# Performance work log

Measured on AMD Instinct MI355X. Metric: run time of the kernel, lower is better.

The kernel has to match this reference:

```python
import jax, jax.numpy as jnp
import numpy as np

SCALE = 20.0
THRESHOLD = 0.9995


def setup_inputs() -> dict:
    key = jax.random.key(0)
    k1, k2, k3 = jax.random.split(key, 3)
    B, C, H, W, S = 4, 128, 96, 128, 1024
    # L2-normalize along channel so the dot product is a true cosine in [-1, 1]
    # (keeps exp(scale * (x - threshold)) numerically sane, as intended by the module).
    def unit(x):
        return x / (jnp.linalg.norm(x, axis=1, keepdims=True) + 1e-8)
    source_feature_map = unit(jax.random.normal(k1, (B, C, H, W), dtype=jnp.float32))
    target_feature_map = unit(jax.random.normal(k2, (B, C, H, W), dtype=jnp.float32))
    source_feature_1D_locations = jax.random.randint(k3, (B, S, 1), 0, H * W, dtype=jnp.int64)
    mask = jnp.ones((B, 1, H, W), dtype=jnp.float32)
    return {
        "source_feature_map": source_feature_map,
        "target_feature_map": target_feature_map,
        "source_feature_1D_locations": source_feature_1D_locations,
        "mask": mask,
    }


def reference(source_feature_map, target_feature_map, source_feature_1D_locations, mask):
    B, C, H, W = source_feature_map.shape
    loc = source_feature_1D_locations[..., 0]  # [B, S]
    src_flat = source_feature_map.reshape(B, C, H * W)  # [B, C, HW]
    # gather sampled query vectors: [B, C, S]
    sampled = jnp.take_along_axis(src_flat, loc[:, None, :], axis=2)
    # per-batch 1x1 conv == batched matmul: [B, S, H, W]
    corr = jnp.einsum('bchw,bcs->bshw', target_feature_map, sampled)
    resp = jnp.exp(SCALE * (0.5 * corr + 0.5 - THRESHOLD)) * mask  # mask broadcasts [B,1,H,W]
    resp = resp / jnp.sum(resp, axis=(2, 3), keepdims=True)
    return resp
```

## Files before the change

### kernel.cpp

```cpp
#include <hip/hip_runtime.h>

typedef unsigned int u32;
typedef unsigned short u16;
typedef short s8v __attribute__((ext_vector_type(8)));
typedef float f16v __attribute__((ext_vector_type(16)));
typedef _Float16 h8 __attribute__((ext_vector_type(8)));

#define NB 4
#define NC 128
#define HW 12288
#define NS 1024

#define EXP_A 10.0f
#define EXP_B (-9.99f)
#define ESCALE 4096.0f

#define TSR 128
#define TP 256
#define NPT (HW/TP)
#define NRT ((NB*NS)/TSR)

__device__ inline u16 f2bf(float f) {
    u32 u = __float_as_uint(f);
    return (u16)((u + 0x7fffu + ((u >> 16) & 1u)) >> 16);
}
__device__ inline float bf2f(u16 h) { return __uint_as_float(((u32)h) << 16); }

__device__ inline void gload_lds16(const void* g, void* l) {
    __builtin_amdgcn_global_load_lds(
        (const __attribute__((address_space(1))) void*)g,
        (__attribute__((address_space(3))) void*)l, 16, 0, 0);
}

__global__ __launch_bounds__(256) void prep(
    const float* __restrict__ src, const float* __restrict__ tgt,
    const int* __restrict__ loc,
    u16* __restrict__ ahi, u16* __restrict__ alo,
    u16* __restrict__ bhi, u16* __restrict__ blo,
    float* __restrict__ sums)
{
    int blk = blockIdx.x, t = threadIdx.x;
    if (blk < (HW / 64) * NB) {
        int b = blk / (HW / 64), pt = blk - b * (HW / 64);
        int pxl = t & 63, u = t >> 6;
        int px = pt * 64 + pxl;
        int slot = u ^ ((px >> 1) & 3);
#pragma unroll
        for (int kc = 0; kc < 4; ++kc) {
            int c0 = kc * 32 + u * 8;
            u32 hq[4], lq[4];
#pragma unroll
            for (int k = 0; k < 4; ++k) {
                float v0 = tgt[((size_t)(b * NC + c0 + 2 * k)) * HW + px];
                float v1 = tgt[((size_t)(b * NC + c0 + 2 * k + 1)) * HW + px];
                u16 h0 = f2bf(v0), h1 = f2bf(v1);
                u16 l0 = f2bf(v0 - bf2f(h0)), l1 = f2bf(v1 - bf2f(h1));
                hq[k] = (u32)h0 | ((u32)h1 << 16);
                lq[k] = (u32)l0 | ((u32)l1 << 16);
            }
            size_t off = (((size_t)((b * 4 + kc) * HW + px)) * 4 + slot) * 8;
            *(uint4*)(bhi + off) = make_uint4(hq[0], hq[1], hq[2], hq[3]);
            *(uint4*)(blo + off) = make_uint4(lq[0], lq[1], lq[2], lq[3]);
        }
    } else {
        int sb = blk - (HW / 64) * NB;
        int gid = sb * 256 + t;
        if (gid < NB * NS) sums[gid] = 0.0f;
        int bs = sb * 2 + (t >> 7);
        int c  = t & 127;
        int b  = bs >> 10, s = bs & 1023;
        int l  = loc[bs];
        float v = src[((size_t)(b * NC + c)) * HW + l];
        u16 h  = f2bf(v);
        u16 lo = f2bf(v - bf2f(h));
        int kc = c >> 5, u = (c >> 3) & 3, e = c & 7;
        int slot = u ^ ((s >> 1) & 3);
        size_t off = ((size_t)((b * 4 + kc) * NS + s)) * 32 + slot * 8 + e;
        ahi[off] = h;
        alo[off] = lo;
    }
}

template <int F16>
__global__ __launch_bounds__(256, 2) void corr_fused(
    const u16* __restrict__ bhi, const u16* __restrict__ blo,
    const u16* __restrict__ ahi, const u16* __restrict__ alo,
    const float* __restrict__ mask, float* __restrict__ sums,
    _Float16* __restrict__ ebuf, float* __restrict__ out)
{
    __shared__ __align__(1024) char sm[49152];

    int f = blockIdx.x;
    int xcd = f & 7, r = f >> 3;
    int pt = xcd * 6 + (r >> 5);
    int rt = r & 31;
    int b  = rt >> 3, st2 = rt & 7;

    int t = threadIdx.x, w = t >> 6, l = t & 63, ln = l & 31, h = l >> 5;
    int ws = w >> 1, wp = w & 1;

    f16v acc[2][4];
#pragma unroll
    for (int i = 0; i < 2; ++i)
#pragma unroll
        for (int j = 0; j < 4; ++j)
#pragma unroll
            for (int r2 = 0; r2 < 16; ++r2) acc[i][j][r2] = 0.0f;

    for (int kc = 0; kc < 4; ++kc) {
        const char* ga_h = (const char*)ahi + ((size_t)((b * 4 + kc) * NS + st2 * TSR)) * 64;
        const char* ga_l = (const char*)alo + ((size_t)((b * 4 + kc) * NS + st2 * TSR)) * 64;
        const char* gb_h = (const char*)bhi + ((size_t)((b * 4 + kc) * HW + pt * TP)) * 64;
        const char* gb_l = (const char*)blo + ((size_t)((b * 4 + kc) * HW + pt * TP)) * 64;
#pragma unroll
        for (int it = 0; it < 12; ++it) {
            int q = w * 12 + it;
            const char* g; int inner;
            if (q < 8)       { g = ga_h; inner = q; }
            else if (q < 16) { g = ga_l; inner = q - 8; }
            else if (q < 32) { g = gb_h; inner = q - 16; }
            else             { g = gb_l; inner = q - 32; }
            gload_lds16(g + inner * 1024 + l * 16, sm + q * 1024);
        }
        __syncthreads();

#pragma unroll
        for (int kk2 = 0; kk2 < 2; ++kk2) {
            int u = kk2 * 2 + h;
            s8v a_h[2], a_l[2], b_h[4], b_l[4];
#pragma unroll
            for (int i = 0; i < 2; ++i) {
                int row = ws * 64 + i * 32 + ln;
                int sl = u ^ ((row >> 1) & 3);
                a_h[i] = *(const s8v*)(sm + 0 * 8192 + row * 64 + sl * 16);
                a_l[i] = *(const s8v*)(sm + 1 * 8192 + row * 64 + sl * 16);
            }
#pragma unroll
            for (int j = 0; j < 4; ++j) {
                int px = wp * 128 + j * 32 + ln;
                int sl = u ^ ((px >> 1) & 3);
                b_h[j] = *(const s8v*)(sm + 16384 + px * 64 + sl * 16);
                b_l[j] = *(const s8v*)(sm + 32768 + px * 64 + sl * 16);
            }
            __builtin_amdgcn_s_setprio(1);
#pragma unroll
            for (int i = 0; i < 2; ++i)
#pragma unroll
                for (int j = 0; j < 4; ++j) {
                    acc[i][j] = __builtin_amdgcn_mfma_f32_32x32x16_bf16(a_h[i], b_h[j], acc[i][j], 0, 0, 0);
                    acc[i][j] = __builtin_amdgcn_mfma_f32_32x32x16_bf16(a_l[i], b_h[j], acc[i][j], 0, 0, 0);
                    acc[i][j] = __builtin_amdgcn_mfma_f32_32x32x16_bf16(a_h[i], b_l[j], acc[i][j], 0, 0, 0);
                }
            __builtin_amdgcn_s_setprio(0);
        }
        __syncthreads();
    }

    float mvs[4];
#pragma unroll
    for (int j = 0; j < 4; ++j)
        mvs[j] = mask[(size_t)b * HW + pt * TP + wp * 128 + j * 32 + ln] * ESCALE;

    float* rs = (float*)sm;
    size_t base = ((size_t)(b * NS + st2 * TSR)) * HW + pt * TP + wp * 128 + ln;
    _Float16* eb0 = ebuf + base;
    float*    ob0 = out  + base;
#pragma unroll
    for (int i = 0; i < 2; ++i) {
        int rb = ws * 64 + i * 32 + 4 * h;
#pragma unroll
        for (int r2 = 0; r2 < 16; ++r2) {
            int row = rb + (r2 & 3) + 8 * (r2 >> 2);
            float tot = 0.0f;
#pragma unroll
            for (int j = 0; j < 4; ++j) {
                float e = __expf(fmaf(acc[i][j][r2], EXP_A, EXP_B)) * mvs[j];
                if (F16) eb0[(size_t)row * HW + j * 32] = (_Float16)e;
                else     ob0[(size_t)row * HW + j * 32] = e;
                tot += e;
            }
            rs[(wp * TSR + row) * 32 + ln] = tot;
        }
    }
    __syncthreads();
    int row2 = t & 127, half = t >> 7;
    float tot = 0.0f;
#pragma unroll
    for (int c = 0; c < 32; ++c)
        tot += rs[(half * TSR + row2) * 32 + ((c + t) & 31)];
    atomicAdd(&sums[b * NS + st2 * TSR + row2], tot);
}

__global__ __launch_bounds__(256) void rescale16(
    const float* __restrict__ sums, const _Float16* __restrict__ ebuf,
    float* __restrict__ out)
{
    int bs = blockIdx.x;
    float inv = 1.0f / sums[bs];
    const h8* p = (const h8*)(ebuf + (size_t)bs * HW);
    float4* o = (float4*)(out + (size_t)bs * HW);
    int t = threadIdx.x;
#pragma unroll
    for (int i = 0; i < 6; ++i) {
        int idx = t + i * 256;
        h8 v = p[idx];
        float4 a, c;
        a.x = (float)v[0] * inv; a.y = (float)v[1] * inv;
        a.z = (float)v[2] * inv; a.w = (float)v[3] * inv;
        c.x = (float)v[4] * inv; c.y = (float)v[5] * inv;
        c.z = (float)v[6] * inv; c.w = (float)v[7] * inv;
        o[2 * idx]     = a;
        o[2 * idx + 1] = c;
    }
}

__global__ __launch_bounds__(256) void rescale32(
    const float* __restrict__ sums, float* __restrict__ out)
{
    int bs = blockIdx.x;
    float inv = 1.0f / sums[bs];
    float4* p = (float4*)(out + (size_t)bs * HW);
    int t = threadIdx.x;
#pragma unroll
    for (int i = 0; i < 12; ++i) {
        float4 v = p[t + i * 256];
        v.x *= inv; v.y *= inv; v.z *= inv; v.w *= inv;
        p[t + i * 256] = v;
    }
}

extern "C" void kernel_launch(void* const* d_in, const int* in_sizes, int n_in,
                              void* d_out, int out_size, void* d_ws, size_t ws_size,
                              hipStream_t stream) {
    const float* src  = (const float*)d_in[0];
    const float* tgt  = (const float*)d_in[1];
    const int*   loc  = (const int*)d_in[2];
    const float* mask = (const float*)d_in[3];
    float* out = (float*)d_out;

    char* ws = (char*)d_ws;
    const size_t BPLANE = (size_t)NB * 4 * HW * 32 * sizeof(u16);
    const size_t APLANE = (size_t)NB * 4 * NS * 32 * sizeof(u16);
    const size_t EPLANE = (size_t)NB * NS * HW * sizeof(_Float16);
    u16* bhi = (u16*)ws;
    u16* blo = (u16*)(ws + BPLANE);
    u16* ahi = (u16*)(ws + 2 * BPLANE);
    u16* alo = (u16*)(ws + 2 * BPLANE + APLANE);
    float* sums = (float*)(ws + 2 * BPLANE + 2 * APLANE);
    _Float16* ebuf = (_Float16*)(ws + 2 * BPLANE + 2 * APLANE + 65536);
    const size_t NEED = 2 * BPLANE + 2 * APLANE + 65536 + EPLANE;

    prep<<<dim3((HW / 64) * NB + NB * NS / 2), 256, 0, stream>>>(
        src, tgt, loc, ahi, alo, bhi, blo, sums);

    dim3 g(NPT * NRT);
    if (ws_size >= NEED) {
        corr_fused<1><<<g, 256, 0, stream>>>(bhi, blo, ahi, alo, mask, sums, ebuf, out);
        rescale16<<<dim3(NB * NS), 256, 0, stream>>>(sums, ebuf, out);
    } else {
        corr_fused<0><<<g, 256, 0, stream>>>(bhi, blo, ahi, alo, mask, sums, ebuf, out);
        rescale32<<<dim3(NB * NS), 256, 0, stream>>>(sums, out);
    }
}
```

Before: 327.8 us.

## Fuse correlation and rescale into one persistent cooperative kernel with grid sync

New measurement: 329.9 us. No clear change (+0.7%).

```diff
diff --git a/kernel.cpp b/kernel.cpp
--- a/kernel.cpp
+++ b/kernel.cpp
@@ -1,4 +1,7 @@
 #include <hip/hip_runtime.h>
+#include <hip/hip_cooperative_groups.h>
+
+namespace cg = cooperative_groups;
 
 typedef unsigned int u32;
 typedef unsigned short u16;
@@ -81,6 +84,143 @@
     }
 }
 
+__global__ __launch_bounds__(256, 2) void corr_norm(
+    const u16* __restrict__ bhi, const u16* __restrict__ blo,
+    const u16* __restrict__ ahi, const u16* __restrict__ alo,
+    const float* __restrict__ mask, float* __restrict__ sums,
+    _Float16* __restrict__ ebuf, float* __restrict__ out)
+{
+    __shared__ __align__(1024) char sm[49152];
+
+    int blk = blockIdx.x;
+    int xcd = blk & 7, idx = blk >> 3;
+    int rt  = idx & 31;
+    int b   = rt >> 3, st2 = rt & 7;
+
+    int t = threadIdx.x, w = t >> 6, l = t & 63, ln = l & 31, h = l >> 5;
+    int ws = w >> 1, wp = w & 1;
+
+    for (int k = 0; k < 3; ++k) {
+        int tid = idx + (k << 6);
+        int pt  = xcd * 6 + (tid >> 5);
+
+        f16v acc[2][4];
+#pragma unroll
+        for (int i = 0; i < 2; ++i)
+#pragma unroll
+            for (int j = 0; j < 4; ++j)
+#pragma unroll
+                for (int r2 = 0; r2 < 16; ++r2) acc[i][j][r2] = 0.0f;
+
+        for (int kc = 0; kc < 4; ++kc) {
+            const char* ga_h = (const char*)ahi + ((size_t)((b * 4 + kc) * NS + st2 * TSR)) * 64;
+            const char* ga_l = (const char*)alo + ((size_t)((b * 4 + kc) * NS + st2 * TSR)) * 64;
+            const char* gb_h = (const char*)bhi + ((size_t)((b * 4 + kc) * HW + pt * TP)) * 64;
+            const char* gb_l = (const char*)blo + ((size_t)((b * 4 + kc) * HW + pt * TP)) * 64;
+#pragma unroll
+            for (int it = 0; it < 12; ++it) {
+                int q = w * 12 + it;
+                const char* g; int inner;
+                if (q < 8)       { g = ga_h; inner = q; }
+                else if (q < 16) { g = ga_l; inner = q - 8; }
+                else if (q < 32) { g = gb_h; inner = q - 16; }
+                else             { g = gb_l; inner = q - 32; }
+                gload_lds16(g + inner * 1024 + l * 16, sm + q * 1024);
+            }
+            __syncthreads();
+
+#pragma unroll
+            for (int kk2 = 0; kk2 < 2; ++kk2) {
+                int u = kk2 * 2 + h;
+                s8v a_h[2], a_l[2], b_h[4], b_l[4];
+#pragma unroll
+                for (int i = 0; i < 2; ++i) {
+                    int row = ws * 64 + i * 32 + ln;
+                    int sl = u ^ ((row >> 1) & 3);
+                    a_h[i] = *(const s8v*)(sm + 0 * 8192 + row * 64 + sl * 16);
+                    a_l[i] = *(const s8v*)(sm + 1 * 8192 + row * 64 + sl * 16);
+                }
+#pragma unroll
+                for (int j = 0; j < 4; ++j) {
+                    int px = wp * 128 + j * 32 + ln;
+                    int sl = u ^ ((px >> 1) & 3);
+                    b_h[j] = *(const s8v*)(sm + 16384 + px * 64 + sl * 16);
+                    b_l[j] = *(const s8v*)(sm + 32768 + px * 64 + sl * 16);
+                }
+                __builtin_amdgcn_s_setprio(1);
+#pragma unroll
+                for (int i = 0; i < 2; ++i)
+#pragma unroll
+                    for (int j = 0; j < 4; ++j) {
+                        acc[i][j] = __builtin_amdgcn_mfma_f32_32x32x16_bf16(a_h[i], b_h[j], acc[i][j], 0, 0, 0);
+                        acc[i][j] = __builtin_amdgcn_mfma_f32_32x32x16_bf16(a_l[i], b_h[j], acc[i][j], 0, 0, 0);
+                        acc[i][j] = __builtin_amdgcn_mfma_f32_32x32x16_bf16(a_h[i], b_l[j], acc[i][j], 0, 0, 0);
+                    }
+                __builtin_amdgcn_s_setprio(0);
+            }
+            __syncthreads();
+        }
+
+        float mvs[4];
+#pragma unroll
+        for (int j = 0; j < 4; ++j)
+            mvs[j] = mask[(size_t)b * HW + pt * TP + wp * 128 + j * 32 + ln] * ESCALE;
+
+        float* rs = (float*)sm;
+        size_t base = ((size_t)(b * NS + st2 * TSR)) * HW + pt * TP + wp * 128 + ln;
+        _Float16* eb0 = ebuf + base;
+#pragma unroll
+        for (int i = 0; i < 2; ++i) {
+            int rb = ws * 64 + i * 32 + 4 * h;
+#pragma unroll
+            for (int r2 = 0; r2 < 16; ++r2) {
+                int row = rb + (r2 & 3) + 8 * (r2 >> 2);
+                float tot = 0.0f;
+#pragma unroll
+                for (int j = 0; j < 4; ++j) {
+                    float e = __expf(fmaf(acc[i][j][r2], EXP_A, EXP_B)) * mvs[j];
+                    eb0[(size_t)row * HW + j * 32] = (_Float16)e;
+                    tot += e;
+                }
+                rs[(wp * TSR + row) * 32 + ln] = tot;
+            }
+        }
+        __syncthreads();
+        int row2 = t & 127, half = t >> 7;
+        float tot = 0.0f;
+#pragma unroll
+        for (int c = 0; c < 32; ++c)
+            tot += rs[(half * TSR + row2) * 32 + ((c + t) & 31)];
+        atomicAdd(&sums[b * NS + st2 * TSR + row2], tot);
+        __syncthreads();
+    }
+
+    __threadfence();
+    cg::this_grid().sync();
+
+    int base_row = blk * 8;
+#pragma unroll
+    for (int k = 0; k < 8; ++k) {
+        int row = base_row + k;
+        float sv = __hip_atomic_load(&sums[row], __ATOMIC_RELAXED, __HIP_MEMORY_SCOPE_AGENT);
+        float inv = 1.0f / sv;
+        const h8* p = (const h8*)(ebuf + (size_t)row * HW);
+        float4* o = (float4*)(out + (size_t)row * HW);
+#pragma unroll
+        for (int i = 0; i < 6; ++i) {
+            int idx2 = t + i * 256;
+            h8 v = p[idx2];
+            float4 a, c;
+            a.x = (float)v[0] * inv; a.y = (float)v[1] * inv;
+            a.z = (float)v[2] * inv; a.w = (float)v[3] * inv;
+            c.x = (float)v[4] * inv; c.y = (float)v[5] * inv;
+            c.z = (float)v[6] * inv; c.w = (float)v[7] * inv;
+            o[2 * idx2]     = a;
+            o[2 * idx2 + 1] = c;
+        }
+    }
+}
+
 template <int F16>
 __global__ __launch_bounds__(256, 2) void corr_fused(
     const u16* __restrict__ bhi, const u16* __restrict__ blo,
@@ -253,12 +393,35 @@
     prep<<<dim3((HW / 64) * NB + NB * NS / 2), 256, 0, stream>>>(
         src, tgt, loc, ahi, alo, bhi, blo, sums);
 
-    dim3 g(NPT * NRT);
+    bool coop_done = false;
     if (ws_size >= NEED) {
-        corr_fused<1><<<g, 256, 0, stream>>>(bhi, blo, ahi, alo, mask, sums, ebuf, out);
-        rescale16<<<dim3(NB * NS), 256, 0, stream>>>(sums, ebuf, out);
-    } else {
-        corr_fused<0><<<g, 256, 0, stream>>>(bhi, blo, ahi, alo, mask, sums, ebuf, out);
-        rescale32<<<dim3(NB * NS), 256, 0, stream>>>(sums, out);
-    }
-}
+        static int coop_state = -1;
+        if (coop_state < 0) {
+            int nb = 0, ncu = 0, dev = 0;
+            hipGetDevice(&dev);
+            hipError_t e1 = hipOccupancyMaxActiveBlocksPerMultiprocessor(
+                &nb, (const void*)corr_norm, 256, 0);
+            hipError_t e2 = hipDeviceGetAttribute(
+                &ncu, hipDeviceAttributeMultiprocessorCount, dev);
+            coop_state = (e1 == hipSuccess && e2 == hipSuccess &&
+                          nb >= 2 && nb * ncu >= 512) ? 1 : 0;
+        }
+        if (coop_state == 1) {
+            void* kargs[] = {(void*)&bhi, (void*)&blo, (void*)&ahi, (void*)&alo,
+                             (void*)&mask, (void*)&sums, (void*)&ebuf, (void*)&out};
+            coop_done = (hipLaunchCooperativeKernel((const void*)corr_norm,
+                          dim3(512), dim3(256), kargs, 0, stream) == hipSuccess);
+        }
+    }
+
+    if (!coop_done) {
+        dim3 g(NPT * NRT);
+        if (ws_size >= NEED) {
+            corr_fused<1><<<g, 256, 0, stream>>>(bhi, blo, ahi, alo, mask, sums, ebuf, out);
+            rescale16<<<dim3(NB * NS), 256, 0, stream>>>(sums, ebuf, out);
+        } else {
+            corr_fused<0><<<g, 256, 0, stream>>>(bhi, blo, ahi, alo, mask, sums, ebuf, out);
+            rescale32<<<dim3(NB * NS), 256, 0, stream>>>(sums, out);
+        }
+    }
+}
```
